# Optimization experiments

Measured on AMD Instinct MI355X. Metric: run time of the kernel, lower is better.

The kernel has to match this reference:

```python
import jax, jax.numpy as jnp
import numpy as np

D, H, O, E, K = 1024, 4096, 1024, 12, 4
N = 8192


def setup_inputs() -> dict:
    key = jax.random.key(0)
    ks = jax.random.split(key, 7)
    s = 0.02
    return {
        "x": jax.random.normal(ks[0], (N, D), dtype=jnp.float32),
        "gate_w": jax.random.normal(ks[1], (D, E), dtype=jnp.float32) * s,
        "gate_b": jnp.zeros((E,), dtype=jnp.float32),
        "w1": jax.random.normal(ks[2], (E, D, H), dtype=jnp.float32) * s,
        "b1": jnp.zeros((E, H), dtype=jnp.float32),
        "w2": jax.random.normal(ks[3], (E, H, O), dtype=jnp.float32) * s,
        "b2": jnp.zeros((E, O), dtype=jnp.float32),
    }


def reference(x, gate_w, gate_b, w1, b1, w2, b2):
    # Gating: full softmax over all experts, then mask to top-k and renormalize
    scores = x @ gate_w + gate_b                      # [N, E]
    _, topk_idx = jax.lax.top_k(scores, K)            # [N, K]
    mask = jnp.sum(jax.nn.one_hot(topk_idx, E, dtype=scores.dtype), axis=-2)  # [N, E]
    weights = jax.nn.softmax(scores, axis=-1) * mask
    weights = weights / (jnp.sum(weights, axis=-1, keepdims=True) + 1e-8)

    # Dense all-expert MLP (faithful to original: every expert on every token)
    h = jax.nn.relu(jnp.einsum("nd,edh->neh", x, w1) + b1)  # [N, E, H]
    outs = jnp.einsum("neh,eho->neo", h, w2) + b2           # [N, E, O]

    return jnp.einsum("ne,neo->no", weights, outs)          # [N, O]
```

## Files before the change

### kernel.cpp

```cpp
#include <hip/hip_runtime.h>
#include <stdint.h>

#define D_DIM 1024
#define H_DIM 4096
#define O_DIM 1024
#define E_NUM 12
#define TOPK 4
#define N_TOK 8192

#define PAIR_CAP 34304

typedef __bf16 bf16x8 __attribute__((ext_vector_type(8)));
typedef float f32x4 __attribute__((ext_vector_type(4)));

typedef __attribute__((address_space(3))) unsigned int lds_uint;
typedef __attribute__((address_space(1))) const unsigned int glob_uint;

static __device__ __forceinline__ unsigned short f2b(float f) {
  union { float f; unsigned u; } v; v.f = f;
  unsigned r = v.u + 0x7FFFu + ((v.u >> 16) & 1u);
  return (unsigned short)(r >> 16);
}

static __device__ __forceinline__ void gload16(const void* g, void* l) {
  __builtin_amdgcn_global_load_lds((glob_uint*)g, (lds_uint*)l, 16, 0, 0);
}

__global__ __launch_bounds__(256) void cvt_x_kernel(const float* __restrict__ x,
                                                    unsigned short* __restrict__ xb) {
  int i = blockIdx.x * 256 + threadIdx.x;
  const float4* p = reinterpret_cast<const float4*>(x);
  float4 a = p[2 * i], b = p[2 * i + 1];
  uint4 st;
  st.x = (unsigned)f2b(a.x) | ((unsigned)f2b(a.y) << 16);
  st.y = (unsigned)f2b(a.z) | ((unsigned)f2b(a.w) << 16);
  st.z = (unsigned)f2b(b.x) | ((unsigned)f2b(b.y) << 16);
  st.w = (unsigned)f2b(b.z) | ((unsigned)f2b(b.w) << 16);
  reinterpret_cast<uint4*>(xb)[i] = st;
}

__global__ __launch_bounds__(256) void transpose_cvt_kernel(const float* __restrict__ in,
                                                            unsigned short* __restrict__ out,
                                                            int R, int C) {
  __shared__ float tile[32][33];
  int e = blockIdx.z;
  size_t base = (size_t)e * R * C;
  int c0 = blockIdx.x * 32, r0 = blockIdx.y * 32;
  int tx = threadIdx.x, ty = threadIdx.y;
#pragma unroll
  for (int i = 0; i < 32; i += 8)
    tile[ty + i][tx] = in[base + (size_t)(r0 + ty + i) * C + (c0 + tx)];
  __syncthreads();
#pragma unroll
  for (int i = 0; i < 32; i += 8)
    out[base + (size_t)(c0 + ty + i) * R + (r0 + tx)] = f2b(tile[tx][ty + i]);
}

__global__ __launch_bounds__(256) void gwt_kernel(const float* __restrict__ gw,
                                                  float* __restrict__ gwT) {
  int e = blockIdx.x;
#pragma unroll
  for (int i = 0; i < 4; i++) {
    int d = i * 256 + threadIdx.x;
    gwT[e * D_DIM + d] = gw[(size_t)d * E_NUM + e];
  }
}

__global__ __launch_bounds__(256) void gating_kernel(const float* __restrict__ x,
                                                     const float* __restrict__ gwT,
                                                     const float* __restrict__ gb,
                                                     int* __restrict__ tk_e,
                                                     float* __restrict__ tk_w) {
  int wv = (blockIdx.x * 256 + threadIdx.x) >> 6;
  int lane = threadIdx.x & 63;
  int n0 = wv * 4;
  if (n0 >= N_TOK) return;

  const float4* x4 = reinterpret_cast<const float4*>(x);
  const float4* g4 = reinterpret_cast<const float4*>(gwT);

  float acc[4][E_NUM];
#pragma unroll
  for (int t = 0; t < 4; t++)
#pragma unroll
    for (int e = 0; e < E_NUM; e++) acc[t][e] = 0.f;

#pragma unroll
  for (int i = 0; i < 4; i++) {
    float4 xv[4];
#pragma unroll
    for (int t = 0; t < 4; t++) xv[t] = x4[(size_t)(n0 + t) * 256 + i * 64 + lane];
#pragma unroll
    for (int e = 0; e < E_NUM; e++) {
      float4 g = g4[e * 256 + i * 64 + lane];
#pragma unroll
      for (int t = 0; t < 4; t++) {
        acc[t][e] += xv[t].x * g.x + xv[t].y * g.y + xv[t].z * g.z + xv[t].w * g.w;
      }
    }
  }

#pragma unroll
  for (int t = 0; t < 4; t++)
#pragma unroll
    for (int e = 0; e < E_NUM; e++) {
      float v = acc[t][e];
#pragma unroll
      for (int s = 32; s > 0; s >>= 1) v += __shfl_xor(v, s, 64);
      acc[t][e] = v;
    }

#pragma unroll
  for (int t = 0; t < 4; t++) {
    if (lane == t) {
      int n = n0 + t;
      float sc[E_NUM], sm[E_NUM];
      float mx = -1e30f;
#pragma unroll
      for (int e = 0; e < E_NUM; e++) { sc[e] = acc[t][e] + gb[e]; mx = fmaxf(mx, sc[e]); }
      float Z = 0.f;
#pragma unroll
      for (int e = 0; e < E_NUM; e++) { sm[e] = expf(sc[e] - mx); Z += sm[e]; }
      bool used[E_NUM];
#pragma unroll
      for (int e = 0; e < E_NUM; e++) used[e] = false;
      int eid[TOPK]; float p[TOPK]; float wsum = 0.f;
      for (int k = 0; k < TOPK; k++) {
        float best = -1e30f; int bi = 0;
        for (int e = 0; e < E_NUM; e++)
          if (!used[e] && sc[e] > best) { best = sc[e]; bi = e; }
        used[bi] = true; eid[k] = bi; p[k] = sm[bi] / Z; wsum += p[k];
      }
      float inv = 1.f / (wsum + 1e-8f);
      for (int k = 0; k < TOPK; k++) {
        tk_e[n * TOPK + k] = eid[k];
        tk_w[n * TOPK + k] = p[k] * inv;
      }
    }
  }
}

__global__ __launch_bounds__(256) void hist_rank_kernel(const int* __restrict__ tk_e,
                                                        int* __restrict__ lr,
                                                        int* __restrict__ bc) {
  int blk = blockIdx.x, t = threadIdx.x;
  int n = blk * 256 + t;
  int4 te = reinterpret_cast<const int4*>(tk_e)[n];
  int lane = t & 63, w = t >> 6;
  __shared__ int wt[4][E_NUM];
  int r0 = 0, r1 = 0, r2 = 0, r3 = 0;
#pragma unroll
  for (int e = 0; e < E_NUM; e++) {
    int flag = (te.x == e) || (te.y == e) || (te.z == e) || (te.w == e);
    unsigned long long m = __ballot(flag);
    int rw = __popcll(m & ((1ull << lane) - 1ull));
    if (lane == 0) wt[w][e] = __popcll(m);
    if (te.x == e) r0 = rw;
    if (te.y == e) r1 = rw;
    if (te.z == e) r2 = rw;
    if (te.w == e) r3 = rw;
  }
  __syncthreads();
#pragma unroll
  for (int e = 0; e < E_NUM; e++) {
    int base = 0;
#pragma unroll
    for (int w2 = 0; w2 < 4; w2++)
      if (w2 < w) base += wt[w2][e];
    if (te.x == e) r0 += base;
    if (te.y == e) r1 += base;
    if (te.z == e) r2 += base;
    if (te.w == e) r3 += base;
  }
  int4 out; out.x = r0; out.y = r1; out.z = r2; out.w = r3;
  reinterpret_cast<int4*>(lr)[n] = out;
  if (t == 0) {
#pragma unroll
    for (int e = 0; e < E_NUM; e++)
      bc[blk * E_NUM + e] = wt[0][e] + wt[1][e] + wt[2][e] + wt[3][e];
  }
}

__global__ __launch_bounds__(64) void scan2_kernel(const int* __restrict__ bc,
                                                   int* __restrict__ poff,
                                                   int* __restrict__ bb) {
  int t = threadIdx.x;
  __shared__ int cnte[E_NUM];
  __shared__ int spoff[E_NUM + 1];
  if (t < E_NUM) {
    int s = 0;
#pragma unroll
    for (int b = 0; b < 32; b++) s += bc[b * E_NUM + t];
    cnte[t] = s;
  }
  __syncthreads();
  if (t == 0) {
    int off = 0; spoff[0] = 0;
    for (int e = 0; e < E_NUM; e++) {
      off += ((cnte[e] + 127) >> 7) << 7;
      spoff[e + 1] = off;
    }
  }
  __syncthreads();
  if (t < E_NUM + 1) poff[t] = spoff[t];
  if (t < E_NUM) {
    int run = spoff[t];
    for (int b = 0; b < 32; b++) {
      bb[b * E_NUM + t] = run;
      run += bc[b * E_NUM + t];
    }
  }
}

__global__ __launch_bounds__(256) void fill_pairs_kernel(int* __restrict__ pt,
                                                         float* __restrict__ pw) {
  int i = blockIdx.x * 256 + threadIdx.x;
  if (i < PAIR_CAP) { pt[i] = 0; pw[i] = 0.f; }
}

__global__ __launch_bounds__(256) void scatter2_kernel(const int* __restrict__ tk_e,
                                                       const float* __restrict__ tk_w,
                                                       const int* __restrict__ lr,
                                                       const int* __restrict__ bb,
                                                       int* __restrict__ pt,
                                                       float* __restrict__ pw) {
  int n = blockIdx.x * 256 + threadIdx.x;
  if (n >= N_TOK) return;
  int blk = n >> 8;
  int4 te = reinterpret_cast<const int4*>(tk_e)[n];
  int4 l4 = reinterpret_cast<const int4*>(lr)[n];
  float4 wv = reinterpret_cast<const float4*>(tk_w)[n];
  int p0 = bb[blk * E_NUM + te.x] + l4.x;
  int p1 = bb[blk * E_NUM + te.y] + l4.y;
  int p2 = bb[blk * E_NUM + te.z] + l4.z;
  int p3 = bb[blk * E_NUM + te.w] + l4.w;
  pt[p0] = n; pw[p0] = wv.x;
  pt[p1] = n; pw[p1] = wv.y;
  pt[p2] = n; pw[p2] = wv.z;
  pt[p3] = n; pw[p3] = wv.w;
}


__global__ __launch_bounds__(256, 2) void gemm1_kernel(
    const unsigned short* __restrict__ xb,
    const unsigned short* __restrict__ w1t,
    const float* __restrict__ b1,
    const int* __restrict__ pair_token,
    const int* __restrict__ poff,
    unsigned short* __restrict__ hbuf,
    int tile0) {
  __shared__ unsigned short As[128 * 32];
  __shared__ unsigned short Bs[128 * 32];
  int t = tile0 + blockIdx.y;
  int totTiles = poff[E_NUM] >> 7;
  if (t >= totTiles) return;
  int rowg0 = t << 7;
  int e = 0;
#pragma unroll
  for (int i = 1; i < E_NUM; i++) e += (rowg0 >= poff[i]);

  const int tid = threadIdx.x;
  const int lane = tid & 63, wave = tid >> 6;
  const int wm = wave >> 1, wn = wave & 1;
  const int fr = lane & 15, fgq = lane >> 4;

  const int srow = tid >> 2;
  const int skc = (((tid & 3) ^ ((srow >> 1) & 3)) << 3);
  int tok0 = pair_token[rowg0 + srow];
  int tok1 = pair_token[rowg0 + 64 + srow];
  const unsigned short* a0 = xb + (size_t)tok0 * D_DIM + skc;
  const unsigned short* a1 = xb + (size_t)tok1 * D_DIM + skc;
  int n0 = blockIdx.x << 7;
  const unsigned short* wb = w1t + (size_t)e * H_DIM * D_DIM;
  const unsigned short* b0p = wb + (size_t)(n0 + srow) * D_DIM + skc;
  const unsigned short* b1p = wb + (size_t)(n0 + 64 + srow) * D_DIM + skc;
  unsigned short* lA0 = &As[tid * 8];
  unsigned short* lA1 = &As[2048 + tid * 8];
  unsigned short* lB0 = &Bs[tid * 8];
  unsigned short* lB1 = &Bs[2048 + tid * 8];

  const int cswz = (fgq ^ ((fr >> 1) & 3)) << 3;
  int aoff[4], boff[4];
#pragma unroll
  for (int mf = 0; mf < 4; mf++) aoff[mf] = (wm * 64 + mf * 16 + fr) * 32 + cswz;
#pragma unroll
  for (int nf = 0; nf < 4; nf++) boff[nf] = (wn * 64 + nf * 16 + fr) * 32 + cswz;

  f32x4 acc[4][4];
#pragma unroll
  for (int i = 0; i < 4; i++)
#pragma unroll
    for (int j = 0; j < 4; j++) acc[i][j] = (f32x4){0.f, 0.f, 0.f, 0.f};

  for (int kt = 0; kt < D_DIM / 32; ++kt) {
    int k0 = kt * 32;
    gload16(a0 + k0, lA0);
    gload16(a1 + k0, lA1);
    gload16(b0p + k0, lB0);
    gload16(b1p + k0, lB1);
    __syncthreads();
    bf16x8 af[4], bq[4];
#pragma unroll
    for (int mf = 0; mf < 4; mf++)
      af[mf] = *reinterpret_cast<const bf16x8*>(&As[aoff[mf]]);
#pragma unroll
    for (int nf = 0; nf < 4; nf++)
      bq[nf] = *reinterpret_cast<const bf16x8*>(&Bs[boff[nf]]);
#pragma unroll
    for (int mf = 0; mf < 4; mf++)
#pragma unroll
      for (int nf = 0; nf < 4; nf++)
        acc[mf][nf] = __builtin_amdgcn_mfma_f32_16x16x32_bf16(af[mf], bq[nf], acc[mf][nf], 0, 0, 0);
    __syncthreads();
  }

  int lrow0 = blockIdx.y << 7;
#pragma unroll
  for (int nf = 0; nf < 4; nf++) {
    int col = n0 + wn * 64 + nf * 16 + fr;
    float bias = b1[e * H_DIM + col];
#pragma unroll
    for (int mf = 0; mf < 4; mf++) {
      int m = wm * 64 + mf * 16 + fgq * 4;
#pragma unroll
      for (int r = 0; r < 4; r++) {
        float v = fmaxf(acc[mf][nf][r] + bias, 0.f);
        hbuf[(size_t)(lrow0 + m + r) * H_DIM + col] = f2b(v);
      }
    }
  }
}

__global__ __launch_bounds__(256, 2) void gemm2_kernel(
    const unsigned short* __restrict__ hbuf,
    const unsigned short* __restrict__ w2t,
    const float* __restrict__ b2,
    const int* __restrict__ pair_token,
    const float* __restrict__ pair_w,
    const int* __restrict__ poff,
    float* __restrict__ out,
    int tile0) {
  __shared__ unsigned short As[128 * 32];
  __shared__ unsigned short Bs[128 * 32];
  int t = tile0 + blockIdx.y;
  int totTiles = poff[E_NUM] >> 7;
  if (t >= totTiles) return;
  int rowg0 = t << 7;
  int e = 0;
#pragma unroll
  for (int i = 1; i < E_NUM; i++) e += (rowg0 >= poff[i]);

  const int tid = threadIdx.x;
  const int lane = tid & 63, wave = tid >> 6;
  const int wm = wave >> 1, wn = wave & 1;
  const int fr = lane & 15, fgq = lane >> 4;
  const int ksplit = blockIdx.z;
  const int kbase = ksplit * (H_DIM / 2);

  const int srow = tid >> 2;
  const int skc = (((tid & 3) ^ ((srow >> 1) & 3)) << 3);
  int lrowb = blockIdx.y << 7;
  const unsigned short* a0 = hbuf + (size_t)(lrowb + srow) * H_DIM + kbase + skc;
  const unsigned short* a1 = hbuf + (size_t)(lrowb + 64 + srow) * H_DIM + kbase + skc;
  int n0 = blockIdx.x << 7;
  const unsigned short* wb = w2t + (size_t)e * O_DIM * H_DIM;
  const unsigned short* b0p = wb + (size_t)(n0 + srow) * H_DIM + kbase + skc;
  const unsigned short* b1p = wb + (size_t)(n0 + 64 + srow) * H_DIM + kbase + skc;
  unsigned short* lA0 = &As[tid * 8];
  unsigned short* lA1 = &As[2048 + tid * 8];
  unsigned short* lB0 = &Bs[tid * 8];
  unsigned short* lB1 = &Bs[2048 + tid * 8];

  const int cswz = (fgq ^ ((fr >> 1) & 3)) << 3;
  int aoff[4], boff[4];
#pragma unroll
  for (int mf = 0; mf < 4; mf++) aoff[mf] = (wm * 64 + mf * 16 + fr) * 32 + cswz;
#pragma unroll
  for (int nf = 0; nf < 4; nf++) boff[nf] = (wn * 64 + nf * 16 + fr) * 32 + cswz;

  f32x4 acc[4][4];
#pragma unroll
  for (int i = 0; i < 4; i++)
#pragma unroll
    for (int j = 0; j < 4; j++) acc[i][j] = (f32x4){0.f, 0.f, 0.f, 0.f};

  for (int kt = 0; kt < H_DIM / 2 / 32; ++kt) {
    int k0 = kt * 32;
    gload16(a0 + k0, lA0);
    gload16(a1 + k0, lA1);
    gload16(b0p + k0, lB0);
    gload16(b1p + k0, lB1);
    __syncthreads();
    bf16x8 af[4], bq[4];
#pragma unroll
    for (int mf = 0; mf < 4; mf++)
      af[mf] = *reinterpret_cast<const bf16x8*>(&As[aoff[mf]]);
#pragma unroll
    for (int nf = 0; nf < 4; nf++)
      bq[nf] = *reinterpret_cast<const bf16x8*>(&Bs[boff[nf]]);
#pragma unroll
    for (int mf = 0; mf < 4; mf++)
#pragma unroll
      for (int nf = 0; nf < 4; nf++)
        acc[mf][nf] = __builtin_amdgcn_mfma_f32_16x16x32_bf16(af[mf], bq[nf], acc[mf][nf], 0, 0, 0);
    __syncthreads();
  }

  int toks[16]; float wts[16];
#pragma unroll
  for (int mf = 0; mf < 4; mf++)
#pragma unroll
    for (int r = 0; r < 4; r++) {
      int grow = rowg0 + wm * 64 + mf * 16 + fgq * 4 + r;
      toks[mf * 4 + r] = pair_token[grow];
      wts[mf * 4 + r] = pair_w[grow];
    }
#pragma unroll
  for (int nf = 0; nf < 4; nf++) {
    int col = n0 + wn * 64 + nf * 16 + fr;
    float bias = (ksplit == 0) ? b2[e * O_DIM + col] : 0.f;
#pragma unroll
    for (int mf = 0; mf < 4; mf++)
#pragma unroll
      for (int r = 0; r < 4; r++) {
        float v = wts[mf * 4 + r] * (acc[mf][nf][r] + bias);
        atomicAdd(&out[(size_t)toks[mf * 4 + r] * O_DIM + col], v);
      }
  }
}

extern "C" void kernel_launch(void* const* d_in, const int* in_sizes, int n_in,
                              void* d_out, int out_size, void* d_ws, size_t ws_size,
                              hipStream_t stream) {
  const float* x  = (const float*)d_in[0];
  const float* gw = (const float*)d_in[1];
  const float* gb = (const float*)d_in[2];
  const float* w1 = (const float*)d_in[3];
  const float* b1 = (const float*)d_in[4];
  const float* w2 = (const float*)d_in[5];
  const float* b2 = (const float*)d_in[6];
  float* out = (float*)d_out;

  char* ws = (char*)d_ws;
  size_t off = 0;
  auto alloc = [&](size_t bytes) -> void* {
    void* p = ws + off;
    off = (off + bytes + 255) & ~(size_t)255;
    return p;
  };
  unsigned short* xb   = (unsigned short*)alloc((size_t)N_TOK * D_DIM * 2);
  unsigned short* w1t  = (unsigned short*)alloc((size_t)E_NUM * H_DIM * D_DIM * 2);
  unsigned short* w2t  = (unsigned short*)alloc((size_t)E_NUM * O_DIM * H_DIM * 2);
  float* gwT  = (float*)alloc((size_t)E_NUM * D_DIM * 4);
  int*   tk_e = (int*)alloc((size_t)N_TOK * TOPK * 4);
  float* tk_w = (float*)alloc((size_t)N_TOK * TOPK * 4);
  int*   lr   = (int*)alloc((size_t)N_TOK * TOPK * 4);
  int*   pt   = (int*)alloc((size_t)PAIR_CAP * 4);
  float* pw   = (float*)alloc((size_t)PAIR_CAP * 4);
  int*   bc   = (int*)alloc(32 * E_NUM * 4);
  int*   bb   = (int*)alloc(32 * E_NUM * 4);
  int*   poff = (int*)alloc(64);

  int TPC, NCH;
  size_t need2 = off + (size_t)134 * 128 * H_DIM * 2 + 256;
  if (ws_size >= need2) { TPC = 134; NCH = 2; }
  else                  { TPC = 67;  NCH = 4; }
  unsigned short* hbuf = (unsigned short*)alloc((size_t)TPC * 128 * H_DIM * 2);
  if (off > ws_size) return;

  hipMemsetAsync(d_out, 0, (size_t)out_size * 4, stream);

  cvt_x_kernel<<<N_TOK * D_DIM / 8 / 256, 256, 0, stream>>>(x, xb);
  transpose_cvt_kernel<<<dim3(H_DIM / 32, D_DIM / 32, E_NUM), dim3(32, 8), 0, stream>>>(w1, w1t, D_DIM, H_DIM);
  transpose_cvt_kernel<<<dim3(O_DIM / 32, H_DIM / 32, E_NUM), dim3(32, 8), 0, stream>>>(w2, w2t, H_DIM, O_DIM);
  gwt_kernel<<<E_NUM, 256, 0, stream>>>(gw, gwT);
  gating_kernel<<<N_TOK / 16, 256, 0, stream>>>(x, gwT, gb, tk_e, tk_w);
  hist_rank_kernel<<<N_TOK / 256, 256, 0, stream>>>(tk_e, lr, bc);
  scan2_kernel<<<1, 64, 0, stream>>>(bc, poff, bb);
  fill_pairs_kernel<<<(PAIR_CAP + 255) / 256, 256, 0, stream>>>(pt, pw);
  scatter2_kernel<<<N_TOK / 256, 256, 0, stream>>>(tk_e, tk_w, lr, bb, pt, pw);

  for (int c = 0; c < NCH; c++) {
    int tile0 = c * TPC;
    gemm1_kernel<<<dim3(H_DIM / 128, TPC), 256, 0, stream>>>(xb, w1t, b1, pt, poff, hbuf, tile0);
    gemm2_kernel<<<dim3(O_DIM / 128, TPC, 2), 256, 0, stream>>>(hbuf, w2t, b2, pt, pw, poff, out, tile0);
  }
}
```

Measured before the change: 1.173 ms.

## Replace gemm2 atomic scatter with bf16 per-pair outputs and a gather reduce

gemm2 now writes unweighted per-pair expert outputs as bf16 into a staging buffer, one slice per K-split, instead of issuing weighted fp32 atomicAdds into the output. A new reduce kernel gathers each token's four pair rows, applies the gating weights and writes the output directly, so the output memset and the pair-weight array are no longer needed. scatter2 stores each token's pair positions in place of the local ranks for the reduce to use. This removes atomic contention and scattered read-modify-write traffic, at the cost of an extra staging buffer, an additional kernel pass and bf16 rounding of intermediate outputs.

```diff
diff --git a/kernel.cpp b/kernel.cpp
--- a/kernel.cpp
+++ b/kernel.cpp
@@ -12,6 +12,7 @@
 
 typedef __bf16 bf16x8 __attribute__((ext_vector_type(8)));
 typedef float f32x4 __attribute__((ext_vector_type(4)));
+typedef unsigned short u16x8 __attribute__((ext_vector_type(8)));
 
 typedef __attribute__((address_space(3))) unsigned int lds_uint;
 typedef __attribute__((address_space(1))) const unsigned int glob_uint;
@@ -212,32 +213,27 @@
   }
 }
 
-__global__ __launch_bounds__(256) void fill_pairs_kernel(int* __restrict__ pt,
-                                                         float* __restrict__ pw) {
+__global__ __launch_bounds__(256) void fill_pairs_kernel(int* __restrict__ pt) {
   int i = blockIdx.x * 256 + threadIdx.x;
-  if (i < PAIR_CAP) { pt[i] = 0; pw[i] = 0.f; }
+  if (i < PAIR_CAP) pt[i] = 0;
 }
 
 __global__ __launch_bounds__(256) void scatter2_kernel(const int* __restrict__ tk_e,
-                                                       const float* __restrict__ tk_w,
-                                                       const int* __restrict__ lr,
+                                                       int* __restrict__ lr_ip,
                                                        const int* __restrict__ bb,
-                                                       int* __restrict__ pt,
-                                                       float* __restrict__ pw) {
+                                                       int* __restrict__ pt) {
   int n = blockIdx.x * 256 + threadIdx.x;
   if (n >= N_TOK) return;
   int blk = n >> 8;
   int4 te = reinterpret_cast<const int4*>(tk_e)[n];
-  int4 l4 = reinterpret_cast<const int4*>(lr)[n];
-  float4 wv = reinterpret_cast<const float4*>(tk_w)[n];
+  int4 l4 = reinterpret_cast<const int4*>(lr_ip)[n];
   int p0 = bb[blk * E_NUM + te.x] + l4.x;
   int p1 = bb[blk * E_NUM + te.y] + l4.y;
   int p2 = bb[blk * E_NUM + te.z] + l4.z;
   int p3 = bb[blk * E_NUM + te.w] + l4.w;
-  pt[p0] = n; pw[p0] = wv.x;
-  pt[p1] = n; pw[p1] = wv.y;
-  pt[p2] = n; pw[p2] = wv.z;
-  pt[p3] = n; pw[p3] = wv.w;
+  pt[p0] = n; pt[p1] = n; pt[p2] = n; pt[p3] = n;
+  int4 ip; ip.x = p0; ip.y = p1; ip.z = p2; ip.w = p3;
+  reinterpret_cast<int4*>(lr_ip)[n] = ip;
 }
 
 
@@ -335,11 +331,9 @@
     const unsigned short* __restrict__ hbuf,
     const unsigned short* __restrict__ w2t,
     const float* __restrict__ b2,
-    const int* __restrict__ pair_token,
-    const float* __restrict__ pair_w,
     const int* __restrict__ poff,
-    float* __restrict__ out,
-    int tile0) {
+    unsigned short* __restrict__ youts,
+    int tile0, int nsplit) {
   __shared__ unsigned short As[128 * 32];
   __shared__ unsigned short Bs[128 * 32];
   int t = tile0 + blockIdx.y;
@@ -354,8 +348,9 @@
   const int lane = tid & 63, wave = tid >> 6;
   const int wm = wave >> 1, wn = wave & 1;
   const int fr = lane & 15, fgq = lane >> 4;
-  const int ksplit = blockIdx.z;
-  const int kbase = ksplit * (H_DIM / 2);
+  const int z = blockIdx.z;
+  const int kspan = H_DIM / nsplit;
+  const int kbase = z * kspan;
 
   const int srow = tid >> 2;
   const int skc = (((tid & 3) ^ ((srow >> 1) & 3)) << 3);
@@ -384,7 +379,7 @@
 #pragma unroll
     for (int j = 0; j < 4; j++) acc[i][j] = (f32x4){0.f, 0.f, 0.f, 0.f};
 
-  for (int kt = 0; kt < H_DIM / 2 / 32; ++kt) {
+  for (int kt = 0; kt < kspan / 32; ++kt) {
     int k0 = kt * 32;
     gload16(a0 + k0, lA0);
     gload16(a1 + k0, lA1);
@@ -406,27 +401,69 @@
     __syncthreads();
   }
 
-  int toks[16]; float wts[16];
-#pragma unroll
-  for (int mf = 0; mf < 4; mf++)
-#pragma unroll
-    for (int r = 0; r < 4; r++) {
-      int grow = rowg0 + wm * 64 + mf * 16 + fgq * 4 + r;
-      toks[mf * 4 + r] = pair_token[grow];
-      wts[mf * 4 + r] = pair_w[grow];
-    }
+  size_t ybase = (size_t)z * PAIR_CAP;
 #pragma unroll
   for (int nf = 0; nf < 4; nf++) {
     int col = n0 + wn * 64 + nf * 16 + fr;
-    float bias = (ksplit == 0) ? b2[e * O_DIM + col] : 0.f;
-#pragma unroll
-    for (int mf = 0; mf < 4; mf++)
+    float bias = (z == 0) ? b2[e * O_DIM + col] : 0.f;
+#pragma unroll
+    for (int mf = 0; mf < 4; mf++) {
+      int m = wm * 64 + mf * 16 + fgq * 4;
 #pragma unroll
       for (int r = 0; r < 4; r++) {
-        float v = wts[mf * 4 + r] * (acc[mf][nf][r] + bias);
-        atomicAdd(&out[(size_t)toks[mf * 4 + r] * O_DIM + col], v);
+        float v = acc[mf][nf][r] + bias;
+        youts[(ybase + rowg0 + m + r) * O_DIM + col] = f2b(v);
       }
-  }
+    }
+  }
+}
+
+static __device__ __forceinline__ void acc8(float* a, const unsigned short* y, float wk) {
+  u16x8 v = *reinterpret_cast<const u16x8*>(y);
+#pragma unroll
+  for (int j = 0; j < 8; j++)
+    a[j] += wk * __uint_as_float((unsigned)v[j] << 16);
+}
+
+__global__ __launch_bounds__(256) void reduce_kernel(const unsigned short* __restrict__ youts,
+                                                     const int* __restrict__ ip,
+                                                     const float* __restrict__ tk_w,
+                                                     float* __restrict__ out,
+                                                     int nsplit) {
+  int gid = blockIdx.x * 256 + threadIdx.x;
+  int n = gid >> 7;
+  int c0 = (gid & 127) << 3;
+  int4 p = reinterpret_cast<const int4*>(ip)[n];
+  float4 w = reinterpret_cast<const float4*>(tk_w)[n];
+  const size_t zoff = (size_t)PAIR_CAP * O_DIM;
+  float a[8];
+#pragma unroll
+  for (int j = 0; j < 8; j++) a[j] = 0.f;
+  {
+    const unsigned short* y = youts + (size_t)p.x * O_DIM + c0;
+    acc8(a, y, w.x);
+    if (nsplit == 2) acc8(a, y + zoff, w.x);
+  }
+  {
+    const unsigned short* y = youts + (size_t)p.y * O_DIM + c0;
+    acc8(a, y, w.y);
+    if (nsplit == 2) acc8(a, y + zoff, w.y);
+  }
+  {
+    const unsigned short* y = youts + (size_t)p.z * O_DIM + c0;
+    acc8(a, y, w.z);
+    if (nsplit == 2) acc8(a, y + zoff, w.z);
+  }
+  {
+    const unsigned short* y = youts + (size_t)p.w * O_DIM + c0;
+    acc8(a, y, w.w);
+    if (nsplit == 2) acc8(a, y + zoff, w.w);
+  }
+  float* orow = out + (size_t)n * O_DIM + c0;
+  float4 o0; o0.x = a[0]; o0.y = a[1]; o0.z = a[2]; o0.w = a[3];
+  float4 o1; o1.x = a[4]; o1.y = a[5]; o1.z = a[6]; o1.w = a[7];
+  reinterpret_cast<float4*>(orow)[0] = o0;
+  reinterpret_cast<float4*>(orow)[1] = o1;
 }
 
 extern "C" void kernel_launch(void* const* d_in, const int* in_sizes, int n_in,
@@ -456,19 +493,20 @@
   float* tk_w = (float*)alloc((size_t)N_TOK * TOPK * 4);
   int*   lr   = (int*)alloc((size_t)N_TOK * TOPK * 4);
   int*   pt   = (int*)alloc((size_t)PAIR_CAP * 4);
-  float* pw   = (float*)alloc((size_t)PAIR_CAP * 4);
   int*   bc   = (int*)alloc(32 * E_NUM * 4);
   int*   bb   = (int*)alloc(32 * E_NUM * 4);
   int*   poff = (int*)alloc(64);
 
-  int TPC, NCH;
-  size_t need2 = off + (size_t)134 * 128 * H_DIM * 2 + 256;
-  if (ws_size >= need2) { TPC = 134; NCH = 2; }
-  else                  { TPC = 67;  NCH = 4; }
-  unsigned short* hbuf = (unsigned short*)alloc((size_t)TPC * 128 * H_DIM * 2);
+  const size_t HB134 = (size_t)134 * 128 * H_DIM * 2;
+  const size_t HB67  = (size_t)67 * 128 * H_DIM * 2;
+  const size_t YO    = (size_t)PAIR_CAP * O_DIM * 2;
+  int TPC, NCH, NS;
+  if (ws_size >= off + HB134 + 2 * YO + 1024)      { TPC = 134; NCH = 2; NS = 2; }
+  else if (ws_size >= off + HB134 + YO + 1024)     { TPC = 134; NCH = 2; NS = 1; }
+  else                                             { TPC = 67;  NCH = 4; NS = 1; }
+  unsigned short* hbuf  = (unsigned short*)alloc((size_t)TPC * 128 * H_DIM * 2);
+  unsigned short* youts = (unsigned short*)alloc((size_t)NS * YO);
   if (off > ws_size) return;
-
-  hipMemsetAsync(d_out, 0, (size_t)out_size * 4, stream);
 
   cvt_x_kernel<<<N_TOK * D_DIM / 8 / 256, 256, 0, stream>>>(x, xb);
   transpose_cvt_kernel<<<dim3(H_DIM / 32, D_DIM / 32, E_NUM), dim3(32, 8), 0, stream>>>(w1, w1t, D_DIM, H_DIM);
@@ -477,12 +515,13 @@
   gating_kernel<<<N_TOK / 16, 256, 0, stream>>>(x, gwT, gb, tk_e, tk_w);
   hist_rank_kernel<<<N_TOK / 256, 256, 0, stream>>>(tk_e, lr, bc);
   scan2_kernel<<<1, 64, 0, stream>>>(bc, poff, bb);
-  fill_pairs_kernel<<<(PAIR_CAP + 255) / 256, 256, 0, stream>>>(pt, pw);
-  scatter2_kernel<<<N_TOK / 256, 256, 0, stream>>>(tk_e, tk_w, lr, bb, pt, pw);
+  fill_pairs_kernel<<<(PAIR_CAP + 255) / 256, 256, 0, stream>>>(pt);
+  scatter2_kernel<<<N_TOK / 256, 256, 0, stream>>>(tk_e, lr, bb, pt);
 
   for (int c = 0; c < NCH; c++) {
     int tile0 = c * TPC;
     gemm1_kernel<<<dim3(H_DIM / 128, TPC), 256, 0, stream>>>(xb, w1t, b1, pt, poff, hbuf, tile0);
-    gemm2_kernel<<<dim3(O_DIM / 128, TPC, 2), 256, 0, stream>>>(hbuf, w2t, b2, pt, pw, poff, out, tile0);
-  }
-}
+    gemm2_kernel<<<dim3(O_DIM / 128, TPC, NS), 256, 0, stream>>>(hbuf, w2t, b2, poff, youts, tile0, NS);
+  }
+  reduce_kernel<<<N_TOK * (O_DIM / 8) / 256, 256, 0, stream>>>(youts, lr, tk_w, out, NS);
+}
```

Result: faster. 1.002 ms (-14.6%).
